# Optimization experiments

Hardware: AMD Instinct MI355X
Metric: run time of the kernel (lower is better)

Reference implementation:

```python
import jax, jax.numpy as jnp
import numpy as np

K = 3        # num patches
S = 2        # scale factor
G = 32       # base glimpse size


def _avg_pool(x, k):
    # x: (b, c, H, W), kernel=stride=k (matches F.avg_pool2d(x, k))
    if k == 1:
        return x
    b, c, h, w = x.shape
    return x.reshape(b, c, h // k, k, w // k, k).mean(axis=(3, 5))


def _extract_patch(x, l, size):
    # x: (b, c, h, w); l: (b, 2) in [-1, 1]; returns (b, c, size, size)
    b, c, h, w = x.shape
    start = (0.5 * ((l + 1.0) * h)).astype(jnp.int32)  # (b, 2) [col, row]
    pad = size // 2 + 1
    xp = jnp.pad(x, ((0, 0), (0, 0), (pad, pad), (pad, pad)))

    def slice_one(img, st):
        # img: (c, hp, wp); st: (2,) -> rows use st[1], cols use st[0]
        return jax.lax.dynamic_slice(img, (0, st[1], st[0]), (c, size, size))

    return jax.vmap(slice_one)(xp, start)


def _foveate(x, l):
    phi = []
    size = G
    for _ in range(K):
        phi.append(_extract_patch(x, l, size))
        size = int(S * size)
    # pool every coarser patch back to GxG, concat on channel, flatten
    phi = [_avg_pool(p, p.shape[-1] // G) for p in phi]
    phi = jnp.concatenate(phi, axis=1)          # (b, K*c, G, G)
    return phi.reshape(phi.shape[0], -1)        # (b, K*c*G*G)


def setup_inputs() -> dict:
    key = jax.random.key(0)
    ks = jax.random.split(key, 10)
    b, c, h, w = 256, 3, 224, 224
    h_g = h_l = 1024
    dim = K * G * G * c  # 9216
    x = jax.random.normal(ks[0], (b, c, h, w), dtype=jnp.float32)
    l_prev = jax.random.uniform(ks[1], (b, 2), dtype=jnp.float32, minval=-1.0, maxval=1.0)
    def lin(k, fan_in, fan_out):
        return jax.random.normal(k, (fan_in, fan_out), dtype=jnp.float32) / np.sqrt(fan_in)
    return {
        "x": x, "l_prev": l_prev,
        "W1": lin(ks[2], dim, h_g), "b1": jnp.zeros((h_g,), jnp.float32),
        "W2": lin(ks[3], 2, h_l),   "b2": jnp.zeros((h_l,), jnp.float32),
        "W3": lin(ks[4], h_g, h_g + h_l), "b3": jnp.zeros((h_g + h_l,), jnp.float32),
        "W4": lin(ks[5], h_l, h_g + h_l), "b4": jnp.zeros((h_g + h_l,), jnp.float32),
    }


def reference(x, l_prev, W1, b1, W2, b2, W3, b3, W4, b4):
    glimpse = _foveate(x, l_prev)                       # (b, K*c*G*G)
    g_out = jax.nn.relu(glimpse @ W1 + b1)              # (b, h_g)
    l_out = jax.nn.relu(l_prev @ W2 + b2)               # (b, h_l)
    what = g_out @ W3 + b3                              # (b, h_g+h_l)
    where = l_out @ W4 + b4                             # (b, h_g+h_l)
    return jax.nn.relu(what + where)
```

## Files before the change

kernel.cpp:

```cpp
#include <hip/hip_runtime.h>

typedef __bf16 bf16_t;
typedef __bf16 bf16x8 __attribute__((ext_vector_type(8)));
typedef float f32x4 __attribute__((ext_vector_type(4)));
typedef unsigned short us4 __attribute__((ext_vector_type(4)));
typedef unsigned short us8 __attribute__((ext_vector_type(8)));

template<int F>
__device__ __forceinline__ void fov_scale(const float* __restrict__ xb,
                                          bf16_t* __restrict__ gb,
                                          int r0, int c0, int base, int count, int kidx)
{
  constexpr float inv = 1.0f / (F * F);
  for (int i = threadIdx.x; i < count; i += 256) {
    const int idx = base + i;
    const int ch  = idx >> 10;
    const int rem = idx & 1023;
    const int gy  = rem >> 5, gx = rem & 31;
    const float* xc = xb + ch * 50176;
    float sum = 0.0f;
    const int rbase = r0 + gy * F, cbase = c0 + gx * F;
#pragma unroll
    for (int dy = 0; dy < F; ++dy) {
      const int rr = rbase + dy;
      if ((unsigned)rr < 224u) {
#pragma unroll
        for (int dx = 0; dx < F; ++dx) {
          const int cc = cbase + dx;
          if ((unsigned)cc < 224u) sum += xc[rr * 224 + cc];
        }
      }
    }
    gb[kidx * 3072 + idx] = (bf16_t)(sum * inv);
  }
}

__global__ __launch_bounds__(256) void foveate_kernel(const float* __restrict__ x,
                                                      const float* __restrict__ l,
                                                      bf16_t* __restrict__ g)
{
  const int b = blockIdx.x;
  const float l0 = l[2 * b], l1 = l[2 * b + 1];
  const int st0 = (int)(0.5f * ((l0 + 1.0f) * 224.0f));
  const int st1 = (int)(0.5f * ((l1 + 1.0f) * 224.0f));
  const float* xb = x + (size_t)b * 3 * 50176;
  bf16_t* gb = g + (size_t)b * 9216;
  const int y = blockIdx.y;
  if (y == 0) {
    fov_scale<1>(xb, gb, st1 - 17, st0 - 17, 0, 3072, 0);
  } else if (y <= 2) {
    fov_scale<2>(xb, gb, st1 - 33, st0 - 33, (y - 1) * 1536, 1536, 1);
  } else {
    fov_scale<4>(xb, gb, st1 - 65, st0 - 65, (y - 3) * 768, 768, 2);
  }
}

template<int BM, int BN, int KCHUNK, int NDIM, int KFULL, int KB1>
__global__ __launch_bounds__(256) void gemm_split(const bf16_t* __restrict__ A,
                                                  const float* __restrict__ Bp0,
                                                  const float* __restrict__ Bp1,
                                                  float* __restrict__ part, int Mdim)
{
  constexpr int WROWS = BM / 4;
  constexpr int SM = WROWS / 16;
  constexpr int SN = BN / 16;
  constexpr int LDA = 36;
  __shared__ unsigned short Al[BM * LDA];
  __shared__ unsigned short Bl[BN * LDA];
  const int t = threadIdx.x;
  const int w = t >> 6, lane = t & 63;
  const int lr = lane & 15, kg = lane >> 4;
  const int bm0 = blockIdx.x * BM, bn0 = blockIdx.y * BN;
  const int ks0 = blockIdx.z * KCHUNK;

  f32x4 acc[SM][SN] = {};

  for (int k0 = 0; k0 < KCHUNK; k0 += 32) {
    const int kbase = ks0 + k0;
#pragma unroll
    for (int i = 0; i < BM / 64; ++i) {
      const int q = t + 256 * i;
      const int m = q >> 2, kb = (q & 3) * 8;
      us8 v = *(const us8*)(A + (size_t)(bm0 + m) * KFULL + kbase + kb);
      *(us4*)(&Al[m * LDA + kb])     = __builtin_shufflevector(v, v, 0, 1, 2, 3);
      *(us4*)(&Al[m * LDA + kb + 4]) = __builtin_shufflevector(v, v, 4, 5, 6, 7);
    }
    {
      const int k = t >> 3, nb = (t & 7) * 8;
      const int gk = kbase + k;
      const float* brow = (gk < KB1) ? (Bp0 + (size_t)gk * NDIM)
                                     : (Bp1 + (size_t)(gk - KB1) * NDIM);
      const float4 f0 = *(const float4*)(brow + bn0 + nb);
      const float4 f1 = *(const float4*)(brow + bn0 + nb + 4);
      const float fs[8] = {f0.x, f0.y, f0.z, f0.w, f1.x, f1.y, f1.z, f1.w};
#pragma unroll
      for (int j = 0; j < 8; ++j)
        Bl[(nb + j) * LDA + k] = __builtin_bit_cast(unsigned short, (bf16_t)fs[j]);
    }
    __syncthreads();
    bf16x8 af[SM], bfr[SN];
#pragma unroll
    for (int sm = 0; sm < SM; ++sm) {
      const unsigned short* p = &Al[(w * WROWS + sm * 16 + lr) * LDA + kg * 8];
      us4 x0 = *(const us4*)p;
      us4 x1 = *(const us4*)(p + 4);
      af[sm] = __builtin_bit_cast(bf16x8, __builtin_shufflevector(x0, x1, 0, 1, 2, 3, 4, 5, 6, 7));
    }
#pragma unroll
    for (int sn = 0; sn < SN; ++sn) {
      const unsigned short* p = &Bl[(sn * 16 + lr) * LDA + kg * 8];
      us4 x0 = *(const us4*)p;
      us4 x1 = *(const us4*)(p + 4);
      bfr[sn] = __builtin_bit_cast(bf16x8, __builtin_shufflevector(x0, x1, 0, 1, 2, 3, 4, 5, 6, 7));
    }
#pragma unroll
    for (int sm = 0; sm < SM; ++sm)
#pragma unroll
      for (int sn = 0; sn < SN; ++sn)
        acc[sm][sn] = __builtin_amdgcn_mfma_f32_16x16x32_bf16(af[sm], bfr[sn], acc[sm][sn], 0, 0, 0);
    __syncthreads();
  }
  float* outp = part + (size_t)blockIdx.z * ((size_t)Mdim * NDIM);
#pragma unroll
  for (int sm = 0; sm < SM; ++sm)
#pragma unroll
    for (int sn = 0; sn < SN; ++sn)
#pragma unroll
      for (int r = 0; r < 4; ++r) {
        const int gm = bm0 + w * WROWS + sm * 16 + kg * 4 + r;
        const int gn = bn0 + sn * 16 + lr;
        outp[(size_t)gm * NDIM + gn] = acc[sm][sn][r];
      }
}

__global__ __launch_bounds__(256) void fuse_mid(const float* __restrict__ part1,
                                                const float* __restrict__ b1,
                                                const float* __restrict__ lprev,
                                                const float* __restrict__ W2,
                                                const float* __restrict__ b2,
                                                bf16_t* __restrict__ A2)
{
  const int idx = blockIdx.x * 256 + threadIdx.x;
  const int row = idx >> 11, col = idx & 2047;
  float s;
  if (col < 1024) {
    s = b1[col];
#pragma unroll
    for (int i = 0; i < 8; ++i) s += part1[i * 262144 + row * 1024 + col];
  } else {
    const int n = col - 1024;
    s = fmaf(lprev[2 * row], W2[n], fmaf(lprev[2 * row + 1], W2[1024 + n], b2[n]));
  }
  A2[idx] = (bf16_t)fmaxf(s, 0.0f);
}

__global__ __launch_bounds__(256) void epilogue2(const float* __restrict__ part2,
                                                 const float* __restrict__ b3,
                                                 const float* __restrict__ b4,
                                                 float* __restrict__ out)
{
  const int idx = blockIdx.x * 256 + threadIdx.x;
  const int col = idx & 2047;
  float s = b3[col] + b4[col];
#pragma unroll
  for (int i = 0; i < 4; ++i) s += part2[i * 524288 + idx];
  out[idx] = fmaxf(s, 0.0f);
}

extern "C" void kernel_launch(void* const* d_in, const int* in_sizes, int n_in,
                              void* d_out, int out_size, void* d_ws, size_t ws_size,
                              hipStream_t stream)
{
  const float* x     = (const float*)d_in[0];
  const float* lprev = (const float*)d_in[1];
  const float* W1    = (const float*)d_in[2];
  const float* b1    = (const float*)d_in[3];
  const float* W2    = (const float*)d_in[4];
  const float* b2    = (const float*)d_in[5];
  const float* W3    = (const float*)d_in[6];
  const float* b3    = (const float*)d_in[7];
  const float* W4    = (const float*)d_in[8];
  const float* b4    = (const float*)d_in[9];
  float* out = (float*)d_out;

  char* ws = (char*)d_ws;
  bf16_t* glimpse = (bf16_t*)ws;
  bf16_t* A2      = (bf16_t*)(ws + 4718592);
  float*  part1   = (float*)(ws + 5767168);
  float*  part2   = (float*)(ws + 14155776);

  foveate_kernel<<<dim3(256, 7), 256, 0, stream>>>(x, lprev, glimpse);
  gemm_split<128, 64, 1152, 1024, 9216, 9216>
      <<<dim3(2, 16, 8), 256, 0, stream>>>(glimpse, W1, W1, part1, 256);
  fuse_mid<<<2048, 256, 0, stream>>>(part1, b1, lprev, W2, b2, A2);
  gemm_split<64, 64, 512, 2048, 2048, 1024>
      <<<dim3(4, 32, 4), 256, 0, stream>>>(A2, W3, W4, part2, 256);
  epilogue2<<<2048, 256, 0, stream>>>(part2, b3, b4, out);
}
```

Baseline: 319.9 us.

## Restructure foveation via shared tile, LDS-free GEMMs with full-M blocks, vectorize epilogues

The foveation kernel now stages one 128x128 region per (batch, channel) in shared memory and derives all three scales from it, instead of re-reading global memory for each scale. The GEMMs drop the LDS staging and instead have 8 waves, each covering 32 rows, load A and B fragments straight from global memory, with B read as strided fp32 columns. One block now spans the whole M=256, so each W element is read once, and the split-K factor is doubled to keep enough blocks. The reduction and epilogue kernels are vectorized to 4 elements per thread. The trade-off is uncoalesced strided B loads with no LDS reuse, plus larger partial buffers to sum.

```diff
diff --git a/kernel.cpp b/kernel.cpp
--- a/kernel.cpp
+++ b/kernel.cpp
@@ -6,128 +6,101 @@
 typedef unsigned short us4 __attribute__((ext_vector_type(4)));
 typedef unsigned short us8 __attribute__((ext_vector_type(8)));
 
-template<int F>
-__device__ __forceinline__ void fov_scale(const float* __restrict__ xb,
-                                          bf16_t* __restrict__ gb,
-                                          int r0, int c0, int base, int count, int kidx)
+__global__ __launch_bounds__(256) void foveate2(const float* __restrict__ x,
+                                                const float* __restrict__ l,
+                                                bf16_t* __restrict__ g)
 {
-  constexpr float inv = 1.0f / (F * F);
-  for (int i = threadIdx.x; i < count; i += 256) {
-    const int idx = base + i;
-    const int ch  = idx >> 10;
-    const int rem = idx & 1023;
-    const int gy  = rem >> 5, gx = rem & 31;
-    const float* xc = xb + ch * 50176;
-    float sum = 0.0f;
-    const int rbase = r0 + gy * F, cbase = c0 + gx * F;
+  __shared__ float R[128 * 128];
+  const int b = blockIdx.x, ch = blockIdx.y;
+  const float l0 = l[2 * b], l1 = l[2 * b + 1];
+  const int st0 = (int)(0.5f * ((l0 + 1.0f) * 224.0f));
+  const int st1 = (int)(0.5f * ((l1 + 1.0f) * 224.0f));
+  const int r0 = st1 - 65, c0 = st0 - 65;
+  const float* xc = x + ((size_t)b * 3 + ch) * 50176;
+
+  for (int it = 0; it < 64; ++it) {
+    const int p = it * 256 + threadIdx.x;
+    const int r = p >> 7, c = p & 127;
+    const int gr = r0 + r, gc = c0 + c;
+    float v = 0.0f;
+    if ((unsigned)gr < 224u && (unsigned)gc < 224u) v = xc[gr * 224 + gc];
+    R[p] = v;
+  }
+  __syncthreads();
+
+  bf16_t* gb = g + (size_t)b * 9216 + ch * 1024;
+  for (int it = 0; it < 4; ++it) {
+    const int q = it * 256 + threadIdx.x;
+    const int gy = q >> 5, gx = q & 31;
+    gb[q] = (bf16_t)R[(48 + gy) * 128 + 48 + gx];
+  }
+  for (int it = 0; it < 4; ++it) {
+    const int q = it * 256 + threadIdx.x;
+    const int gy = q >> 5, gx = q & 31;
+    const int base = (32 + 2 * gy) * 128 + 32 + 2 * gx;
+    const float s = R[base] + R[base + 1] + R[base + 128] + R[base + 129];
+    gb[3072 + q] = (bf16_t)(s * 0.25f);
+  }
+  for (int it = 0; it < 4; ++it) {
+    const int q = it * 256 + threadIdx.x;
+    const int gy = q >> 5, gx = q & 31;
+    float s = 0.0f;
 #pragma unroll
-    for (int dy = 0; dy < F; ++dy) {
-      const int rr = rbase + dy;
-      if ((unsigned)rr < 224u) {
-#pragma unroll
-        for (int dx = 0; dx < F; ++dx) {
-          const int cc = cbase + dx;
-          if ((unsigned)cc < 224u) sum += xc[rr * 224 + cc];
-        }
-      }
+    for (int dy = 0; dy < 4; ++dy) {
+      const f32x4 v = *(const f32x4*)&R[(4 * gy + dy) * 128 + 4 * gx];
+      s += v[0] + v[1] + v[2] + v[3];
     }
-    gb[kidx * 3072 + idx] = (bf16_t)(sum * inv);
+    gb[6144 + q] = (bf16_t)(s * 0.0625f);
   }
 }
 
-__global__ __launch_bounds__(256) void foveate_kernel(const float* __restrict__ x,
-                                                      const float* __restrict__ l,
-                                                      bf16_t* __restrict__ g)
+template<int WAVES, int BN, int KCHUNK, int NDIM, int KFULL, int KB1>
+__global__ __launch_bounds__(WAVES * 64) void gemm_direct(const bf16_t* __restrict__ A,
+                                                          const float* __restrict__ Bp0,
+                                                          const float* __restrict__ Bp1,
+                                                          float* __restrict__ part)
 {
-  const int b = blockIdx.x;
-  const float l0 = l[2 * b], l1 = l[2 * b + 1];
-  const int st0 = (int)(0.5f * ((l0 + 1.0f) * 224.0f));
-  const int st1 = (int)(0.5f * ((l1 + 1.0f) * 224.0f));
-  const float* xb = x + (size_t)b * 3 * 50176;
-  bf16_t* gb = g + (size_t)b * 9216;
-  const int y = blockIdx.y;
-  if (y == 0) {
-    fov_scale<1>(xb, gb, st1 - 17, st0 - 17, 0, 3072, 0);
-  } else if (y <= 2) {
-    fov_scale<2>(xb, gb, st1 - 33, st0 - 33, (y - 1) * 1536, 1536, 1);
-  } else {
-    fov_scale<4>(xb, gb, st1 - 65, st0 - 65, (y - 3) * 768, 768, 2);
-  }
-}
-
-template<int BM, int BN, int KCHUNK, int NDIM, int KFULL, int KB1>
-__global__ __launch_bounds__(256) void gemm_split(const bf16_t* __restrict__ A,
-                                                  const float* __restrict__ Bp0,
-                                                  const float* __restrict__ Bp1,
-                                                  float* __restrict__ part, int Mdim)
-{
-  constexpr int WROWS = BM / 4;
-  constexpr int SM = WROWS / 16;
+  constexpr int SM = 2;
   constexpr int SN = BN / 16;
-  constexpr int LDA = 36;
-  __shared__ unsigned short Al[BM * LDA];
-  __shared__ unsigned short Bl[BN * LDA];
-  const int t = threadIdx.x;
-  const int w = t >> 6, lane = t & 63;
+  constexpr int M = WAVES * 32;
+  const int t = threadIdx.x, w = t >> 6, lane = t & 63;
   const int lr = lane & 15, kg = lane >> 4;
-  const int bm0 = blockIdx.x * BM, bn0 = blockIdx.y * BN;
+  const int bn0 = blockIdx.y * BN;
   const int ks0 = blockIdx.z * KCHUNK;
+  const int m0 = w * 32;
 
   f32x4 acc[SM][SN] = {};
-
+#pragma unroll 2
   for (int k0 = 0; k0 < KCHUNK; k0 += 32) {
     const int kbase = ks0 + k0;
+    const float* brow = (kbase < KB1) ? (Bp0 + (size_t)kbase * NDIM)
+                                      : (Bp1 + (size_t)(kbase - KB1) * NDIM);
+    bf16x8 af[SM];
 #pragma unroll
-    for (int i = 0; i < BM / 64; ++i) {
-      const int q = t + 256 * i;
-      const int m = q >> 2, kb = (q & 3) * 8;
-      us8 v = *(const us8*)(A + (size_t)(bm0 + m) * KFULL + kbase + kb);
-      *(us4*)(&Al[m * LDA + kb])     = __builtin_shufflevector(v, v, 0, 1, 2, 3);
-      *(us4*)(&Al[m * LDA + kb + 4]) = __builtin_shufflevector(v, v, 4, 5, 6, 7);
-    }
-    {
-      const int k = t >> 3, nb = (t & 7) * 8;
-      const int gk = kbase + k;
-      const float* brow = (gk < KB1) ? (Bp0 + (size_t)gk * NDIM)
-                                     : (Bp1 + (size_t)(gk - KB1) * NDIM);
-      const float4 f0 = *(const float4*)(brow + bn0 + nb);
-      const float4 f1 = *(const float4*)(brow + bn0 + nb + 4);
-      const float fs[8] = {f0.x, f0.y, f0.z, f0.w, f1.x, f1.y, f1.z, f1.w};
-#pragma unroll
-      for (int j = 0; j < 8; ++j)
-        Bl[(nb + j) * LDA + k] = __builtin_bit_cast(unsigned short, (bf16_t)fs[j]);
-    }
-    __syncthreads();
-    bf16x8 af[SM], bfr[SN];
-#pragma unroll
-    for (int sm = 0; sm < SM; ++sm) {
-      const unsigned short* p = &Al[(w * WROWS + sm * 16 + lr) * LDA + kg * 8];
-      us4 x0 = *(const us4*)p;
-      us4 x1 = *(const us4*)(p + 4);
-      af[sm] = __builtin_bit_cast(bf16x8, __builtin_shufflevector(x0, x1, 0, 1, 2, 3, 4, 5, 6, 7));
-    }
+    for (int sm = 0; sm < SM; ++sm)
+      af[sm] = __builtin_bit_cast(bf16x8,
+          *(const us8*)(A + (size_t)(m0 + sm * 16 + lr) * KFULL + kbase + kg * 8));
+    bf16x8 bfr[SN];
 #pragma unroll
     for (int sn = 0; sn < SN; ++sn) {
-      const unsigned short* p = &Bl[(sn * 16 + lr) * LDA + kg * 8];
-      us4 x0 = *(const us4*)p;
-      us4 x1 = *(const us4*)(p + 4);
-      bfr[sn] = __builtin_bit_cast(bf16x8, __builtin_shufflevector(x0, x1, 0, 1, 2, 3, 4, 5, 6, 7));
+      const float* bp = brow + (size_t)(kg * 8) * NDIM + bn0 + sn * 16 + lr;
+#pragma unroll
+      for (int j = 0; j < 8; ++j) bfr[sn][j] = (bf16_t)bp[(size_t)j * NDIM];
     }
 #pragma unroll
     for (int sm = 0; sm < SM; ++sm)
 #pragma unroll
       for (int sn = 0; sn < SN; ++sn)
         acc[sm][sn] = __builtin_amdgcn_mfma_f32_16x16x32_bf16(af[sm], bfr[sn], acc[sm][sn], 0, 0, 0);
-    __syncthreads();
   }
-  float* outp = part + (size_t)blockIdx.z * ((size_t)Mdim * NDIM);
+  float* outp = part + (size_t)blockIdx.z * ((size_t)M * NDIM);
 #pragma unroll
   for (int sm = 0; sm < SM; ++sm)
 #pragma unroll
     for (int sn = 0; sn < SN; ++sn)
 #pragma unroll
       for (int r = 0; r < 4; ++r) {
-        const int gm = bm0 + w * WROWS + sm * 16 + kg * 4 + r;
+        const int gm = m0 + sm * 16 + kg * 4 + r;
         const int gn = bn0 + sn * 16 + lr;
         outp[(size_t)gm * NDIM + gn] = acc[sm][sn][r];
       }
@@ -140,18 +113,25 @@
                                                 const float* __restrict__ b2,
                                                 bf16_t* __restrict__ A2)
 {
-  const int idx = blockIdx.x * 256 + threadIdx.x;
-  const int row = idx >> 11, col = idx & 2047;
-  float s;
+  const int e = (blockIdx.x * 256 + threadIdx.x) * 4;
+  const int row = e >> 11, col = e & 2047;
+  f32x4 s;
   if (col < 1024) {
-    s = b1[col];
+    s = *(const f32x4*)(b1 + col);
 #pragma unroll
-    for (int i = 0; i < 8; ++i) s += part1[i * 262144 + row * 1024 + col];
+    for (int z = 0; z < 16; ++z)
+      s += *(const f32x4*)(part1 + (size_t)z * 262144 + row * 1024 + col);
   } else {
     const int n = col - 1024;
-    s = fmaf(lprev[2 * row], W2[n], fmaf(lprev[2 * row + 1], W2[1024 + n], b2[n]));
+    const f32x4 w0 = *(const f32x4*)(W2 + n);
+    const f32x4 w1 = *(const f32x4*)(W2 + 1024 + n);
+    s = *(const f32x4*)(b2 + n) + lprev[2 * row] * w0 + lprev[2 * row + 1] * w1;
   }
-  A2[idx] = (bf16_t)fmaxf(s, 0.0f);
+  us4 o;
+#pragma unroll
+  for (int j = 0; j < 4; ++j)
+    o[j] = __builtin_bit_cast(unsigned short, (bf16_t)fmaxf(s[j], 0.0f));
+  *(us4*)(A2 + e) = o;
 }
 
 __global__ __launch_bounds__(256) void epilogue2(const float* __restrict__ part2,
@@ -159,12 +139,16 @@
                                                  const float* __restrict__ b4,
                                                  float* __restrict__ out)
 {
-  const int idx = blockIdx.x * 256 + threadIdx.x;
-  const int col = idx & 2047;
-  float s = b3[col] + b4[col];
+  const int e = (blockIdx.x * 256 + threadIdx.x) * 4;
+  const int col = e & 2047;
+  f32x4 s = *(const f32x4*)(b3 + col) + *(const f32x4*)(b4 + col);
 #pragma unroll
-  for (int i = 0; i < 4; ++i) s += part2[i * 524288 + idx];
-  out[idx] = fmaxf(s, 0.0f);
+  for (int z = 0; z < 8; ++z)
+    s += *(const f32x4*)(part2 + (size_t)z * 524288 + e);
+  f32x4 o;
+#pragma unroll
+  for (int j = 0; j < 4; ++j) o[j] = fmaxf(s[j], 0.0f);
+  *(f32x4*)(out + e) = o;
 }
 
 extern "C" void kernel_launch(void* const* d_in, const int* in_sizes, int n_in,
@@ -187,13 +171,13 @@
   bf16_t* glimpse = (bf16_t*)ws;
   bf16_t* A2      = (bf16_t*)(ws + 4718592);
   float*  part1   = (float*)(ws + 5767168);
-  float*  part2   = (float*)(ws + 14155776);
+  float*  part2   = (float*)(ws + 22544384);
 
-  foveate_kernel<<<dim3(256, 7), 256, 0, stream>>>(x, lprev, glimpse);
-  gemm_split<128, 64, 1152, 1024, 9216, 9216>
-      <<<dim3(2, 16, 8), 256, 0, stream>>>(glimpse, W1, W1, part1, 256);
-  fuse_mid<<<2048, 256, 0, stream>>>(part1, b1, lprev, W2, b2, A2);
-  gemm_split<64, 64, 512, 2048, 2048, 1024>
-      <<<dim3(4, 32, 4), 256, 0, stream>>>(A2, W3, W4, part2, 256);
-  epilogue2<<<2048, 256, 0, stream>>>(part2, b3, b4, out);
+  foveate2<<<dim3(256, 3), 256, 0, stream>>>(x, lprev, glimpse);
+  gemm_direct<8, 64, 576, 1024, 9216, 9216>
+      <<<dim3(1, 16, 16), 512, 0, stream>>>(glimpse, W1, W1, part1);
+  fuse_mid<<<512, 256, 0, stream>>>(part1, b1, lprev, W2, b2, A2);
+  gemm_direct<8, 64, 256, 2048, 2048, 1024>
+      <<<dim3(1, 32, 8), 512, 0, stream>>>(A2, W3, W4, part2);
+  epilogue2<<<512, 256, 0, stream>>>(part2, b3, b4, out);
 }
```

Result: slower. 327.4 us (+2.3%).
